# Kernel optimization log

Measured on AMD Instinct MI355X. Metric: run time of the kernel, lower is better.

The kernel has to match this reference:

```python
import jax, jax.numpy as jnp
import numpy as np

DIM = 384
HEADS = 6
HIDDEN = int(DIM * 4.0)
SQRT_2_OVER_PI = float(np.sqrt(2.0 / np.pi))
LN_EPS = 1e-5


def gelu_tanh(x):
    return 0.5 * x * (1.0 + jnp.tanh(SQRT_2_OVER_PI * (x + 0.044715 * x ** 3)))


def layer_norm(x, g, b):
    m = jnp.mean(x, axis=-1, keepdims=True)
    v = jnp.var(x, axis=-1, keepdims=True)
    return (x - m) * jax.lax.rsqrt(v + LN_EPS) * g + b


def setup_inputs() -> dict:
    key = jax.random.key(0)
    ks = jax.random.split(key, 8)
    s = 0.02
    return {
        "x": jax.random.normal(ks[0], (4, 2048, DIM), dtype=jnp.float32),
        "ln1_g": jnp.ones((DIM,), jnp.float32),
        "ln1_b": jnp.zeros((DIM,), jnp.float32),
        "w_qkv": jax.random.normal(ks[1], (DIM, 3 * DIM), jnp.float32) * s,
        "w_proj": jax.random.normal(ks[2], (DIM, DIM), jnp.float32) * s,
        "b_proj": jnp.zeros((DIM,), jnp.float32),
        "ln2_g": jnp.ones((DIM,), jnp.float32),
        "ln2_b": jnp.zeros((DIM,), jnp.float32),
        "w_fc1": jax.random.normal(ks[3], (DIM, HIDDEN), jnp.float32) * s,
        "b_fc1": jnp.zeros((HIDDEN,), jnp.float32),
        "w_fc2": jax.random.normal(ks[4], (HIDDEN, DIM), jnp.float32) * s,
        "b_fc2": jnp.zeros((DIM,), jnp.float32),
    }


def reference(x, ln1_g, ln1_b, w_qkv, w_proj, b_proj, ln2_g, ln2_b, w_fc1, b_fc1, w_fc2, b_fc2):
    B, N, C = x.shape
    H = HEADS
    Dh = C // H
    scale = Dh ** -0.5

    # Attention (pre-norm)
    h = layer_norm(x, ln1_g, ln1_b)
    qkv = (h @ w_qkv).reshape(B, N, 3, H, Dh)
    q = qkv[:, :, 0].transpose(0, 2, 1, 3)  # [B,H,N,Dh]
    k = qkv[:, :, 1].transpose(0, 2, 1, 3)
    v = qkv[:, :, 2].transpose(0, 2, 1, 3)
    attn = jnp.einsum('bhnd,bhmd->bhnm', q, k) * scale
    attn = jax.nn.softmax(attn, axis=-1)
    o = jnp.einsum('bhnm,bhmd->bhnd', attn, v)
    o = o.transpose(0, 2, 1, 3).reshape(B, N, C)
    x = x + (o @ w_proj + b_proj)

    # MLP (pre-norm)
    h = layer_norm(x, ln2_g, ln2_b)
    h = gelu_tanh(h @ w_fc1 + b_fc1)
    x = x + (h @ w_fc2 + b_fc2)
    return x
```

## Files before the change

### kernel.cpp

```cpp
#include <hip/hip_runtime.h>
#include <math.h>

#define DIM 384
#define HEADS 6
#define DH 64
#define HIDDEN 1536
#define SEQ 2048
#define NTOK 8192
#define LN_EPS 1e-5f
#define S2PI 0.7978845608028654f
#define KPAD 72

typedef __attribute__((ext_vector_type(8))) short short8;
typedef __attribute__((ext_vector_type(4))) float f32x4;
typedef __attribute__((ext_vector_type(4))) unsigned short ushort4v;
typedef __attribute__((ext_vector_type(8))) unsigned short ushort8v;

__device__ __forceinline__ unsigned short f2bf(float f) {
    union { float f; unsigned u; } v; v.f = f;
    unsigned r = v.u + 0x7FFFu + ((v.u >> 16) & 1u);
    return (unsigned short)(r >> 16);
}

__device__ __forceinline__ float bf2f(unsigned short u) {
    union { unsigned u; float f; } v; v.u = ((unsigned)u) << 16;
    return v.f;
}

__device__ __forceinline__ float gelu_tanh(float v) {
    float t = tanhf(S2PI * (v + 0.044715f * v * v * v));
    return 0.5f * v * (1.f + t);
}

__device__ __forceinline__ void gload16(const unsigned short* g, unsigned short* l) {
    __builtin_amdgcn_global_load_lds(
        (const __attribute__((address_space(1))) unsigned int*)g,
        (__attribute__((address_space(3))) unsigned int*)l, 16, 0, 0);
}

__global__ __launch_bounds__(256) void ln_kernel(const float* __restrict__ x,
                                                 const float* __restrict__ g,
                                                 const float* __restrict__ b,
                                                 unsigned short* __restrict__ out) {
    int row  = blockIdx.x * 4 + (threadIdx.x >> 6);
    int lane = threadIdx.x & 63;
    const float* xr = x + (size_t)row * DIM;
    float v[6];
    float s = 0.f, sq = 0.f;
#pragma unroll
    for (int j = 0; j < 6; ++j) {
        v[j] = xr[lane + 64 * j];
        s += v[j];
        sq += v[j] * v[j];
    }
#pragma unroll
    for (int o = 32; o; o >>= 1) {
        s  += __shfl_xor(s, o);
        sq += __shfl_xor(sq, o);
    }
    float mean = s * (1.f / DIM);
    float var  = sq * (1.f / DIM) - mean * mean;
    float rs   = rsqrtf(var + LN_EPS);
    unsigned short* orow = out + (size_t)row * DIM;
#pragma unroll
    for (int j = 0; j < 6; ++j) {
        int c = lane + 64 * j;
        orow[c] = f2bf((v[j] - mean) * rs * g[c] + b[c]);
    }
}

__global__ __launch_bounds__(256) void transpose_w(const float* __restrict__ w,
                                                   unsigned short* __restrict__ wt,
                                                   int K, int N) {
    __shared__ unsigned short t[32][36];
    const int n0 = blockIdx.x * 32, k0 = blockIdx.y * 32;
    const int tid = threadIdx.x;
    {
        int r = tid >> 3, c4 = (tid & 7) * 4;
        float4 v = *reinterpret_cast<const float4*>(&w[(size_t)(k0 + r) * N + n0 + c4]);
        t[c4 + 0][r] = f2bf(v.x);
        t[c4 + 1][r] = f2bf(v.y);
        t[c4 + 2][r] = f2bf(v.z);
        t[c4 + 3][r] = f2bf(v.w);
    }
    __syncthreads();
    {
        int n = tid >> 3, kk = (tid & 7) * 4;
        ushort4v o = { t[n][kk], t[n][kk + 1], t[n][kk + 2], t[n][kk + 3] };
        *reinterpret_cast<ushort4v*>(&wt[(size_t)(n0 + n) * K + k0 + kk]) = o;
    }
}

template <int EPI, int BN>
__global__ __launch_bounds__(256) void mfma_gemm(const unsigned short* __restrict__ A,
                                                 const unsigned short* __restrict__ Bt,
                                                 const float* __restrict__ bias,
                                                 const float* __restrict__ resid,
                                                 float* __restrict__ Cf,
                                                 unsigned short* __restrict__ Cb,
                                                 unsigned short* __restrict__ Qh,
                                                 unsigned short* __restrict__ Kh,
                                                 unsigned short* __restrict__ Vth,
                                                 int M, int N, int K) {
    constexpr int NF = BN / 32;
    __shared__ __align__(16) unsigned short smem[EPI == 0 ? 17408 : (128 * 64 + BN * 64)];
    unsigned short* As = smem;
    unsigned short* Bs = smem + 128 * 64;

    const int tid = threadIdx.x;
    const int wave = tid >> 6, lane = tid & 63;
    const int lg = lane >> 4, lrr = lane & 15;
    const int wr = wave >> 1, wc = wave & 1;
    const int bm = blockIdx.y * 128, bn = blockIdx.x * BN;

    f32x4 acc[4][NF];
    const f32x4 fzero = {0.f, 0.f, 0.f, 0.f};
#pragma unroll
    for (int m = 0; m < 4; ++m)
#pragma unroll
        for (int n = 0; n < NF; ++n) acc[m][n] = fzero;

    const int grow = wave * 8 + (lane >> 3);
    const int gcol = (lane & 7) * 8;
    const unsigned short* apl = A  + (size_t)(bm + grow) * K + gcol;
    const unsigned short* bpl = Bt + (size_t)(bn + grow) * K + gcol;

    for (int k0 = 0; k0 < K; k0 += 64) {
        __syncthreads();
#pragma unroll
        for (int i = 0; i < 4; ++i)
            gload16(apl + (size_t)(i * 32) * K + k0, As + i * 2048 + wave * 512);
#pragma unroll
        for (int i = 0; i < NF; ++i)
            gload16(bpl + (size_t)(i * 32) * K + k0, Bs + i * 2048 + wave * 512);
        __syncthreads();
#pragma unroll
        for (int s = 0; s < 2; ++s) {
            short8 af[4], bf[NF];
#pragma unroll
            for (int m = 0; m < 4; ++m)
                af[m] = *reinterpret_cast<const short8*>(
                    &As[(wr * 64 + m * 16 + lrr) * 64 + s * 32 + lg * 8]);
#pragma unroll
            for (int n = 0; n < NF; ++n)
                bf[n] = *reinterpret_cast<const short8*>(
                    &Bs[(wc * (BN / 2) + n * 16 + lrr) * 64 + s * 32 + lg * 8]);
#pragma unroll
            for (int m = 0; m < 4; ++m)
#pragma unroll
                for (int n = 0; n < NF; ++n)
                    acc[m][n] = __builtin_amdgcn_mfma_f32_16x16x32_bf16(af[m], bf[n], acc[m][n], 0, 0, 0);
        }
    }

    if (EPI == 1) {
#pragma unroll
        for (int m = 0; m < 4; ++m)
#pragma unroll
            for (int j = 0; j < 4; ++j) {
                int row = bm + wr * 64 + m * 16 + lg * 4 + j;
#pragma unroll
                for (int n = 0; n < NF; ++n) {
                    int col = bn + wc * (BN / 2) + n * 16 + lrr;
                    size_t off = (size_t)row * N + col;
                    Cf[off] = acc[m][n][j] + bias[col] + resid[off];
                }
            }
    } else if (EPI == 2) {
#pragma unroll
        for (int m = 0; m < 4; ++m)
#pragma unroll
            for (int j = 0; j < 4; ++j) {
                int row = bm + wr * 64 + m * 16 + lg * 4 + j;
#pragma unroll
                for (int n = 0; n < NF; ++n) {
                    int col = bn + wc * (BN / 2) + n * 16 + lrr;
                    Cb[(size_t)row * N + col] = f2bf(gelu_tanh(acc[m][n][j] + bias[col]));
                }
            }
    } else {
        const int sec = bn / DIM;
        if (sec < 2) {
            unsigned short* dst = (sec == 0) ? Qh : Kh;
#pragma unroll
            for (int m = 0; m < 4; ++m)
#pragma unroll
                for (int j = 0; j < 4; ++j) {
                    int token = bm + wr * 64 + m * 16 + lg * 4 + j;
                    int bb = token >> 11, nn = token & (SEQ - 1);
#pragma unroll
                    for (int n = 0; n < NF; ++n) {
                        int n_glob = bn + wc * (BN / 2) + n * 16 + lrr;
                        int head = (n_glob - sec * DIM) >> 6;
                        int d = n_glob & 63;
                        dst[((size_t)(bb * HEADS + head) * SEQ + nn) * DH + d] =
                            f2bf(acc[m][n][j]);
                    }
                }
        } else {
            __syncthreads();
            unsigned short* T = smem;
#pragma unroll
            for (int m = 0; m < 4; ++m)
#pragma unroll
                for (int n = 0; n < NF; ++n) {
                    int dl = wc * (BN / 2) + n * 16 + lrr;
#pragma unroll
                    for (int j = 0; j < 4; ++j) {
                        int tl = wr * 64 + m * 16 + lg * 4 + j;
                        T[dl * 136 + tl] = f2bf(acc[m][n][j]);
                    }
                }
            __syncthreads();
            int dl = tid >> 1, th = (tid & 1) * 64;
            int dg = bn - 2 * DIM + dl;
            int head = dg >> 6, dd = dg & 63;
            int bb = bm >> 11, nn0 = (bm & (SEQ - 1)) + th;
            unsigned short* dst = &Vth[((size_t)(bb * HEADS + head) * DH + dd) * SEQ + nn0];
#pragma unroll
            for (int i = 0; i < 64; i += 8)
                *reinterpret_cast<ushort8v*>(dst + i) =
                    *reinterpret_cast<const ushort8v*>(&T[dl * 136 + th + i]);
        }
    }
}

__global__ __launch_bounds__(256) void attn_mfma_kernel(const unsigned short* __restrict__ Qh,
                                                        const unsigned short* __restrict__ Kh,
                                                        const unsigned short* __restrict__ Vth,
                                                        unsigned short* __restrict__ out) {
    const int bid = blockIdx.x;
    const int orig = (bid & 7) * 96 + (bid >> 3);
    const int qt = orig & 31;
    const int bh = orig >> 5;
    const int b = bh / HEADS, h = bh % HEADS;
    const int tid = threadIdx.x;
    const int wave = tid >> 6, lane = tid & 63;
    const int lg = lane >> 4;
    const int lrr = lane & 15;

    __shared__ __align__(16) unsigned short Ks[64][KPAD];
    __shared__ __align__(16) unsigned short Vs[64][KPAD];
    __shared__ __align__(16) unsigned short Ps[4][16][KPAD];

    const size_t qkbase = (size_t)bh * SEQ * DH;
    const size_t vbase  = (size_t)bh * DH * SEQ;

    short8 qfrag[2];
    {
        const unsigned short* qp =
            Qh + qkbase + (size_t)(qt * 64 + wave * 16 + lrr) * DH + lg * 8;
        qfrag[0] = *(const short8*)qp;
        qfrag[1] = *(const short8*)(qp + 32);
#pragma unroll
        for (int s = 0; s < 2; ++s)
#pragma unroll
            for (int i = 0; i < 8; ++i)
                qfrag[s][i] = (short)f2bf(bf2f((unsigned short)qfrag[s][i]) * 0.125f);
    }

    float lsum[4];
    f32x4 oacc[4];
    const f32x4 fzero = {0.f, 0.f, 0.f, 0.f};
#pragma unroll
    for (int j = 0; j < 4; ++j) lsum[j] = 0.f;
#pragma unroll
    for (int n = 0; n < 4; ++n) oacc[n] = fzero;

    const int sr = tid >> 2;
    const int sc = (tid & 3) * 16;

    const unsigned short* kp = Kh + qkbase + (size_t)sr * DH + sc;
    const unsigned short* vp = Vth + vbase + (size_t)sr * SEQ + sc;
    short8 rk0 = *(const short8*)kp;
    short8 rk1 = *(const short8*)(kp + 8);
    short8 rv0 = *(const short8*)vp;
    short8 rv1 = *(const short8*)(vp + 8);

    const int NT = SEQ / 64;
    for (int kt = 0; kt < NT; ++kt) {
        *(short8*)&Ks[sr][sc]     = rk0;
        *(short8*)&Ks[sr][sc + 8] = rk1;
        *(short8*)&Vs[sr][sc]     = rv0;
        *(short8*)&Vs[sr][sc + 8] = rv1;
        if (kt + 1 < NT) {
            kp += 64 * DH;
            vp += 64;
            rk0 = *(const short8*)kp;
            rk1 = *(const short8*)(kp + 8);
            rv0 = *(const short8*)vp;
            rv1 = *(const short8*)(vp + 8);
        }
        asm volatile("s_waitcnt lgkmcnt(0)" ::: "memory");
        __builtin_amdgcn_s_barrier();
        __builtin_amdgcn_sched_barrier(0);

        f32x4 sacc[4];
#pragma unroll
        for (int ct = 0; ct < 4; ++ct) sacc[ct] = fzero;
        __builtin_amdgcn_s_setprio(1);
#pragma unroll
        for (int ct = 0; ct < 4; ++ct) {
#pragma unroll
            for (int s = 0; s < 2; ++s) {
                short8 kf = *(const short8*)&Ks[ct * 16 + lrr][s * 32 + lg * 8];
                sacc[ct] = __builtin_amdgcn_mfma_f32_16x16x32_bf16(qfrag[s], kf, sacc[ct], 0, 0, 0);
            }
        }
        __builtin_amdgcn_s_setprio(0);

#pragma unroll
        for (int ct = 0; ct < 4; ++ct)
#pragma unroll
            for (int j = 0; j < 4; ++j) {
                float p = __expf(sacc[ct][j]);
                sacc[ct][j] = p;
                lsum[j] += p;
                Ps[wave][lg * 4 + j][ct * 16 + lrr] = f2bf(p);
            }

        short8 pf0 = *(const short8*)&Ps[wave][lrr][lg * 8];
        short8 pf1 = *(const short8*)&Ps[wave][lrr][32 + lg * 8];
        __builtin_amdgcn_s_setprio(1);
#pragma unroll
        for (int n = 0; n < 4; ++n) {
            short8 vf0 = *(const short8*)&Vs[n * 16 + lrr][lg * 8];
            oacc[n] = __builtin_amdgcn_mfma_f32_16x16x32_bf16(pf0, vf0, oacc[n], 0, 0, 0);
            short8 vf1 = *(const short8*)&Vs[n * 16 + lrr][32 + lg * 8];
            oacc[n] = __builtin_amdgcn_mfma_f32_16x16x32_bf16(pf1, vf1, oacc[n], 0, 0, 0);
        }
        __builtin_amdgcn_s_setprio(0);
        __builtin_amdgcn_s_barrier();
    }

    const int orow0 = qt * 64 + wave * 16 + lg * 4;
#pragma unroll
    for (int j = 0; j < 4; ++j) {
        float ls = lsum[j];
        ls += __shfl_xor(ls, 1);
        ls += __shfl_xor(ls, 2);
        ls += __shfl_xor(ls, 4);
        ls += __shfl_xor(ls, 8);
        float inv = 1.f / ls;
        size_t rowoff = ((size_t)b * SEQ + orow0 + j) * DIM + h * DH + lrr;
#pragma unroll
        for (int n = 0; n < 4; ++n)
            out[rowoff + n * 16] = f2bf(oacc[n][j] * inv);
    }
}

extern "C" void kernel_launch(void* const* d_in, const int* in_sizes, int n_in,
                              void* d_out, int out_size, void* d_ws, size_t ws_size,
                              hipStream_t stream) {
    const float* x      = (const float*)d_in[0];
    const float* ln1_g  = (const float*)d_in[1];
    const float* ln1_b  = (const float*)d_in[2];
    const float* w_qkv  = (const float*)d_in[3];
    const float* w_proj = (const float*)d_in[4];
    const float* b_proj = (const float*)d_in[5];
    const float* ln2_g  = (const float*)d_in[6];
    const float* ln2_b  = (const float*)d_in[7];
    const float* w_fc1  = (const float*)d_in[8];
    const float* b_fc1  = (const float*)d_in[9];
    const float* w_fc2  = (const float*)d_in[10];
    const float* b_fc2  = (const float*)d_in[11];
    float* out = (float*)d_out;

    unsigned short* h_bf   = (unsigned short*)d_ws;
    unsigned short* Qh     = h_bf + (size_t)NTOK * DIM;
    unsigned short* Kh     = Qh + (size_t)NTOK * DIM;
    unsigned short* Vth    = Kh + (size_t)NTOK * DIM;
    unsigned short* fc1_bf = Vth + (size_t)NTOK * DIM;
    unsigned short* wqkv_t = fc1_bf + (size_t)NTOK * HIDDEN;
    unsigned short* wproj_t = wqkv_t + (size_t)DIM * 3 * DIM;
    unsigned short* wfc1_t  = wproj_t + (size_t)DIM * DIM;
    unsigned short* wfc2_t  = wfc1_t + (size_t)DIM * HIDDEN;
    unsigned short* attn_bf = h_bf;
    unsigned short* h2_bf   = Qh;

    transpose_w<<<dim3(3 * DIM / 32, DIM / 32), 256, 0, stream>>>(w_qkv, wqkv_t, DIM, 3 * DIM);
    transpose_w<<<dim3(DIM / 32, DIM / 32), 256, 0, stream>>>(w_proj, wproj_t, DIM, DIM);
    transpose_w<<<dim3(HIDDEN / 32, DIM / 32), 256, 0, stream>>>(w_fc1, wfc1_t, DIM, HIDDEN);
    transpose_w<<<dim3(DIM / 32, HIDDEN / 32), 256, 0, stream>>>(w_fc2, wfc2_t, HIDDEN, DIM);

    ln_kernel<<<NTOK / 4, 256, 0, stream>>>(x, ln1_g, ln1_b, h_bf);

    mfma_gemm<0, 128><<<dim3(3 * DIM / 128, NTOK / 128), 256, 0, stream>>>(
        h_bf, wqkv_t, nullptr, nullptr, nullptr, nullptr, Qh, Kh, Vth,
        NTOK, 3 * DIM, DIM);

    attn_mfma_kernel<<<(SEQ / 64) * 4 * HEADS, 256, 0, stream>>>(
        Qh, Kh, Vth, attn_bf);

    mfma_gemm<1, 64><<<dim3(DIM / 64, NTOK / 128), 256, 0, stream>>>(
        attn_bf, wproj_t, b_proj, x, out, nullptr, nullptr, nullptr, nullptr,
        NTOK, DIM, DIM);

    ln_kernel<<<NTOK / 4, 256, 0, stream>>>(out, ln2_g, ln2_b, h2_bf);

    mfma_gemm<2, 128><<<dim3(HIDDEN / 128, NTOK / 128), 256, 0, stream>>>(
        h2_bf, wfc1_t, b_fc1, nullptr, nullptr, fc1_bf, nullptr, nullptr, nullptr,
        NTOK, HIDDEN, DIM);

    mfma_gemm<1, 64><<<dim3(DIM / 64, NTOK / 128), 256, 0, stream>>>(
        fc1_bf, wfc2_t, b_fc2, out, out, nullptr, nullptr, nullptr, nullptr,
        NTOK, DIM, HIDDEN);
}
```

Before: 256.3 us.

## Merge prep kernels, use exp2 softmax, fast GELU, and transposed QK^T MFMA

Result: faster. 234.5 us (-8.5%).

```diff
diff --git a/kernel.cpp b/kernel.cpp
--- a/kernel.cpp
+++ b/kernel.cpp
@@ -1,4 +1,5 @@
 #include <hip/hip_runtime.h>
+#include <hip/hip_bf16.h>
 #include <math.h>
 
 #define DIM 384
@@ -16,6 +17,17 @@
 typedef __attribute__((ext_vector_type(4))) unsigned short ushort4v;
 typedef __attribute__((ext_vector_type(8))) unsigned short ushort8v;
 
+#if __has_builtin(__builtin_amdgcn_exp2f)
+#define EXP2(x) __builtin_amdgcn_exp2f(x)
+#else
+#define EXP2(x) exp2f(x)
+#endif
+#if __has_builtin(__builtin_amdgcn_rcpf)
+#define RCPF(x) __builtin_amdgcn_rcpf(x)
+#else
+#define RCPF(x) (1.f / (x))
+#endif
+
 __device__ __forceinline__ unsigned short f2bf(float f) {
     union { float f; unsigned u; } v; v.f = f;
     unsigned r = v.u + 0x7FFFu + ((v.u >> 16) & 1u);
@@ -27,9 +39,10 @@
     return v.f;
 }
 
-__device__ __forceinline__ float gelu_tanh(float v) {
-    float t = tanhf(S2PI * (v + 0.044715f * v * v * v));
-    return 0.5f * v * (1.f + t);
+__device__ __forceinline__ float gelu_fast(float v) {
+    float u = S2PI * (v + 0.044715f * v * v * v);
+    float e = EXP2(u * 2.8853900817779268f);
+    return v * (1.f - RCPF(1.f + e));
 }
 
 __device__ __forceinline__ void gload16(const unsigned short* g, unsigned short* l) {
@@ -38,12 +51,13 @@
         (__attribute__((address_space(3))) unsigned int*)l, 16, 0, 0);
 }
 
-__global__ __launch_bounds__(256) void ln_kernel(const float* __restrict__ x,
-                                                 const float* __restrict__ g,
-                                                 const float* __restrict__ b,
-                                                 unsigned short* __restrict__ out) {
-    int row  = blockIdx.x * 4 + (threadIdx.x >> 6);
-    int lane = threadIdx.x & 63;
+__device__ __forceinline__ void ln_body(const float* __restrict__ x,
+                                        const float* __restrict__ g,
+                                        const float* __restrict__ b,
+                                        unsigned short* __restrict__ out,
+                                        int blk, int tid) {
+    int row  = blk * 4 + (tid >> 6);
+    int lane = tid & 63;
     const float* xr = x + (size_t)row * DIM;
     float v[6];
     float s = 0.f, sq = 0.f;
@@ -69,12 +83,11 @@
     }
 }
 
-__global__ __launch_bounds__(256) void transpose_w(const float* __restrict__ w,
-                                                   unsigned short* __restrict__ wt,
-                                                   int K, int N) {
-    __shared__ unsigned short t[32][36];
-    const int n0 = blockIdx.x * 32, k0 = blockIdx.y * 32;
-    const int tid = threadIdx.x;
+__device__ __forceinline__ void tr_body(const float* __restrict__ w,
+                                        unsigned short* __restrict__ wt,
+                                        int K, int N, int bx, int by,
+                                        unsigned short (*t)[36], int tid) {
+    const int n0 = bx * 32, k0 = by * 32;
     {
         int r = tid >> 3, c4 = (tid & 7) * 4;
         float4 v = *reinterpret_cast<const float4*>(&w[(size_t)(k0 + r) * N + n0 + c4]);
@@ -89,6 +102,39 @@
         ushort4v o = { t[n][kk], t[n][kk + 1], t[n][kk + 2], t[n][kk + 3] };
         *reinterpret_cast<ushort4v*>(&wt[(size_t)(n0 + n) * K + k0 + kk]) = o;
     }
+}
+
+__global__ __launch_bounds__(256) void prep_kernel(const float* __restrict__ x,
+                                                   const float* __restrict__ g1,
+                                                   const float* __restrict__ b1,
+                                                   unsigned short* __restrict__ h_bf,
+                                                   const float* __restrict__ w_qkv,
+                                                   unsigned short* __restrict__ wqkv_t,
+                                                   const float* __restrict__ w_proj,
+                                                   unsigned short* __restrict__ wproj_t,
+                                                   const float* __restrict__ w_fc1,
+                                                   unsigned short* __restrict__ wfc1_t,
+                                                   const float* __restrict__ w_fc2,
+                                                   unsigned short* __restrict__ wfc2_t) {
+    __shared__ unsigned short t[32][36];
+    const int tid = threadIdx.x;
+    int bid = blockIdx.x;
+    if (bid < 2048) { ln_body(x, g1, b1, h_bf, bid, tid); return; }
+    bid -= 2048;
+    if (bid < 432) { tr_body(w_qkv, wqkv_t, DIM, 3 * DIM, bid % 36, bid / 36, t, tid); return; }
+    bid -= 432;
+    if (bid < 144) { tr_body(w_proj, wproj_t, DIM, DIM, bid % 12, bid / 12, t, tid); return; }
+    bid -= 144;
+    if (bid < 576) { tr_body(w_fc1, wfc1_t, DIM, HIDDEN, bid % 48, bid / 48, t, tid); return; }
+    bid -= 576;
+    tr_body(w_fc2, wfc2_t, HIDDEN, DIM, bid % 12, bid / 12, t, tid);
+}
+
+__global__ __launch_bounds__(256) void ln_kernel(const float* __restrict__ x,
+                                                 const float* __restrict__ g,
+                                                 const float* __restrict__ b,
+                                                 unsigned short* __restrict__ out) {
+    ln_body(x, g, b, out, blockIdx.x, threadIdx.x);
 }
 
 template <int EPI, int BN>
@@ -175,7 +221,7 @@
 #pragma unroll
                 for (int n = 0; n < NF; ++n) {
                     int col = bn + wc * (BN / 2) + n * 16 + lrr;
-                    Cb[(size_t)row * N + col] = f2bf(gelu_tanh(acc[m][n][j] + bias[col]));
+                    Cb[(size_t)row * N + col] = f2bf(gelu_fast(acc[m][n][j] + bias[col]));
                 }
             }
     } else {
@@ -256,14 +302,12 @@
         for (int s = 0; s < 2; ++s)
 #pragma unroll
             for (int i = 0; i < 8; ++i)
-                qfrag[s][i] = (short)f2bf(bf2f((unsigned short)qfrag[s][i]) * 0.125f);
-    }
-
-    float lsum[4];
+                qfrag[s][i] = (short)f2bf(bf2f((unsigned short)qfrag[s][i]) * 0.18033688011112042f);
+    }
+
+    float lsum = 0.f;
     f32x4 oacc[4];
     const f32x4 fzero = {0.f, 0.f, 0.f, 0.f};
-#pragma unroll
-    for (int j = 0; j < 4; ++j) lsum[j] = 0.f;
 #pragma unroll
     for (int n = 0; n < 4; ++n) oacc[n] = fzero;
 
@@ -304,20 +348,25 @@
 #pragma unroll
             for (int s = 0; s < 2; ++s) {
                 short8 kf = *(const short8*)&Ks[ct * 16 + lrr][s * 32 + lg * 8];
-                sacc[ct] = __builtin_amdgcn_mfma_f32_16x16x32_bf16(qfrag[s], kf, sacc[ct], 0, 0, 0);
+                sacc[ct] = __builtin_amdgcn_mfma_f32_16x16x32_bf16(kf, qfrag[s], sacc[ct], 0, 0, 0);
             }
         }
         __builtin_amdgcn_s_setprio(0);
 
 #pragma unroll
-        for (int ct = 0; ct < 4; ++ct)
-#pragma unroll
-            for (int j = 0; j < 4; ++j) {
-                float p = __expf(sacc[ct][j]);
-                sacc[ct][j] = p;
-                lsum[j] += p;
-                Ps[wave][lg * 4 + j][ct * 16 + lrr] = f2bf(p);
-            }
+        for (int ct = 0; ct < 4; ++ct) {
+            float p0 = EXP2(sacc[ct][0]);
+            float p1 = EXP2(sacc[ct][1]);
+            float p2 = EXP2(sacc[ct][2]);
+            float p3 = EXP2(sacc[ct][3]);
+            lsum += (p0 + p1) + (p2 + p3);
+            union { __hip_bfloat162 h2; unsigned u; } w0, w1;
+            w0.h2 = __float22bfloat162_rn(float2{p0, p1});
+            w1.h2 = __float22bfloat162_rn(float2{p2, p3});
+            unsigned long long dw = (unsigned long long)w0.u |
+                                    ((unsigned long long)w1.u << 32);
+            *reinterpret_cast<unsigned long long*>(&Ps[wave][lrr][ct * 16 + lg * 4]) = dw;
+        }
 
         short8 pf0 = *(const short8*)&Ps[wave][lrr][lg * 8];
         short8 pf1 = *(const short8*)&Ps[wave][lrr][32 + lg * 8];
@@ -333,15 +382,15 @@
         __builtin_amdgcn_s_barrier();
     }
 
+    float ls = lsum;
+    ls += __shfl_xor(ls, 16);
+    ls += __shfl_xor(ls, 32);
+    float linv = 1.f / ls;
+
     const int orow0 = qt * 64 + wave * 16 + lg * 4;
 #pragma unroll
     for (int j = 0; j < 4; ++j) {
-        float ls = lsum[j];
-        ls += __shfl_xor(ls, 1);
-        ls += __shfl_xor(ls, 2);
-        ls += __shfl_xor(ls, 4);
-        ls += __shfl_xor(ls, 8);
-        float inv = 1.f / ls;
+        float inv = __shfl(linv, lg * 4 + j);
         size_t rowoff = ((size_t)b * SEQ + orow0 + j) * DIM + h * DH + lrr;
 #pragma unroll
         for (int n = 0; n < 4; ++n)
@@ -378,12 +427,9 @@
     unsigned short* attn_bf = h_bf;
     unsigned short* h2_bf   = Qh;
 
-    transpose_w<<<dim3(3 * DIM / 32, DIM / 32), 256, 0, stream>>>(w_qkv, wqkv_t, DIM, 3 * DIM);
-    transpose_w<<<dim3(DIM / 32, DIM / 32), 256, 0, stream>>>(w_proj, wproj_t, DIM, DIM);
-    transpose_w<<<dim3(HIDDEN / 32, DIM / 32), 256, 0, stream>>>(w_fc1, wfc1_t, DIM, HIDDEN);
-    transpose_w<<<dim3(DIM / 32, HIDDEN / 32), 256, 0, stream>>>(w_fc2, wfc2_t, HIDDEN, DIM);
-
-    ln_kernel<<<NTOK / 4, 256, 0, stream>>>(x, ln1_g, ln1_b, h_bf);
+    prep_kernel<<<3776, 256, 0, stream>>>(x, ln1_g, ln1_b, h_bf,
+                                          w_qkv, wqkv_t, w_proj, wproj_t,
+                                          w_fc1, wfc1_t, w_fc2, wfc2_t);
 
     mfma_gemm<0, 128><<<dim3(3 * DIM / 128, NTOK / 128), 256, 0, stream>>>(
         h_bf, wqkv_t, nullptr, nullptr, nullptr, nullptr, Qh, Kh, Vth,
```
